# Kernel tuning notes

Measured on AMD Instinct MI355X. Metric: run time of the kernel, lower is better.

Reference implementation:

```python
import jax, jax.numpy as jnp
import numpy as np

N = 20000       # total atoms
E = 320000      # edges (avg degree 16)
F = 128         # num_features
R = 32          # num_radial
NB = 3          # num_blocks
CUTOFF = 5.0
MAX_Z = 37      # max_atomic_number + 1
MIN_DIST = 0.3
PI = 3.141592653589793


def swish(x):
    return x * jax.nn.sigmoid(x)


def sph_harm_l2(rhat):
    # Real spherical harmonics lmax=2, e3nn ordering, 'component' normalization.
    x, y, z = rhat[:, 0], rhat[:, 1], rhat[:, 2]
    s3, s5, s15 = 1.7320508075688772, 2.23606797749979, 3.872983346207417
    sh1 = jnp.stack([s3 * y, s3 * z, s3 * x], axis=-1)                    # l=1 (odd)
    sh2 = jnp.stack([s15 * x * y, s15 * y * z, 0.5 * s5 * (3.0 * z * z - 1.0),
                     s15 * z * x, 0.5 * s15 * (x * x - y * y)], axis=-1)  # l=2 (even)
    return sh1, sh2


def setup_inputs() -> dict:
    key = jax.random.key(0)
    ks = jax.random.split(key, 16)
    rn = lambda k, shape, scale: jax.random.normal(k, shape, dtype=jnp.float32) * scale
    inp = {}
    inp["z"] = jax.random.randint(ks[0], (N,), 0, MAX_Z)
    inp["pos"] = rn(ks[1], (N, 3), 3.0)
    inp["edge_index"] = jax.random.randint(ks[2], (2, E), 0, N)
    # embedding params
    inp["emb_table"] = rn(ks[3], (MAX_Z, F), 1.0)
    inp["emb_W"] = rn(ks[4], (F, F), F ** -0.5)
    inp["emb_b"] = jnp.zeros((F,), jnp.float32)
    # trainable Bessel frequencies (init n*pi, as in bessel RBF)
    inp["bessel_freq"] = jnp.arange(1, R + 1, dtype=jnp.float32) * PI
    # per-block params, stacked over NB blocks
    inp["Wf1"] = rn(ks[5], (NB, R, F), R ** -0.5)
    inp["bf1"] = jnp.zeros((NB, F), jnp.float32)
    inp["Wf2"] = rn(ks[6], (NB, F, 4 * F), F ** -0.5)
    inp["Wsrc"] = rn(ks[7], (NB, F, F), F ** -0.5)
    inp["Wu"] = rn(ks[8], (NB, F, 3 * F), F ** -0.5)
    inp["W1o"] = rn(ks[9], (NB, F, F), F ** -0.5)
    inp["W1e"] = rn(ks[10], (NB, F, F), F ** -0.5)
    inp["W2e"] = rn(ks[11], (NB, F, F), F ** -0.5)
    inp["Wup"] = rn(ks[12], (NB, 4 * F, F), (4 * F) ** -0.5)
    return inp


def forward(z, pos, edge_index, emb_table, emb_W, emb_b, bessel_freq,
            Wf1, bf1, Wf2, Wsrc, Wu, W1o, W1e, W2e, Wup):
    i, j = edge_index[0], edge_index[1]
    rij = pos[j] - pos[i]                                   # [E,3]
    r = jnp.sqrt(jnp.sum(rij * rij, axis=-1) + 1e-12)       # [E]
    rhat = rij / (r[:, None] + 1e-6)
    # mask replaces the edge filtering (min_distance and radius cutoff)
    edge_mask = ((r >= MIN_DIST) & (r < CUTOFF)).astype(pos.dtype)
    sh1, sh2 = sph_harm_l2(rhat)                            # [E,3], [E,5]
    # trainable Bessel RBF with cosine cutoff envelope
    fc = 0.5 * (jnp.cos(PI * r / CUTOFF) + 1.0) * edge_mask
    rbf = jnp.sqrt(2.0 / CUTOFF) * jnp.sin(bessel_freq[None, :] * r[:, None] / CUTOFF) / (r[:, None] + 1e-6)
    rbf = rbf * fc[:, None]                                 # [E,R]
    # atom embedding
    S = swish(emb_table[z] @ emb_W + emb_b)                 # [N,F]
    T = jnp.zeros((N, 11, F), S.dtype)                      # 1o(3)+1e(3)+2e(5) x F channels
    for b in range(NB):
        # radial filter network -> per-edge gates
        w = swish(rbf @ Wf1[b] + bf1[b]) @ Wf2[b]           # [E,4F]
        w = w * edge_mask[:, None]
        wS, w1, w2, w3 = jnp.split(w, 4, axis=-1)
        Sj = S[j]                                           # [E,F] gather
        # scalar messages
        mS = wS * swish(Sj @ Wsrc[b])                       # [E,F]
        aggS = jax.ops.segment_sum(mS, i, num_segments=N)   # [N,F]
        # equivariant messages: sh(l) outer-product edge features
        u1, u2, u3 = jnp.split(Sj @ Wu[b], 3, axis=-1)
        m1o = sh1[:, :, None] * (w1 * u1)[:, None, :]       # [E,3,F]
        m1e = sh1[:, :, None] * (w2 * u2)[:, None, :]       # [E,3,F]
        m2e = sh2[:, :, None] * (w3 * u3)[:, None, :]       # [E,5,F]
        mT = jnp.concatenate([m1o, m1e, m2e], axis=1)       # [E,11,F]
        aggT = jax.ops.segment_sum(mT, i, num_segments=N)   # [N,11,F] scatter-add
        Tin = T + aggT
        # per-irrep channel mixing (self-interaction)
        T1o = jnp.einsum('nmf,fg->nmg', Tin[:, 0:3], W1o[b])
        T1e = jnp.einsum('nmf,fg->nmg', Tin[:, 3:6], W1e[b])
        T2e = jnp.einsum('nmf,fg->nmg', Tin[:, 6:11], W2e[b])
        T = jnp.concatenate([T1o, T1e, T2e], axis=1)
        # invariant norms of each irrep feed back into scalar track
        inv = jnp.concatenate([jnp.sum(T1o * T1o, 1), jnp.sum(T1e * T1e, 1),
                               jnp.sum(T2e * T2e, 1)], axis=-1)   # [N,3F]
        S = S + swish(jnp.concatenate([aggS, inv], axis=-1) @ Wup[b])
    return S, T.reshape(N, 11 * F)


def reference(z, pos, edge_index, emb_table, emb_W, emb_b, bessel_freq,
              Wf1, bf1, Wf2, Wsrc, Wu, W1o, W1e, W2e, Wup):
    return forward(z, pos, edge_index, emb_table, emb_W, emb_b, bessel_freq,
                   Wf1, bf1, Wf2, Wsrc, Wu, W1o, W1e, W2e, Wup)
```

## Files before the change

### kernel.cpp

```cpp
#include <hip/hip_runtime.h>
#include <cstdint>
#include <cstddef>

#define NN 20000
#define EE 320000
#define FF 128
#define RR 32
#define MTE 16

typedef float  f32x4  __attribute__((ext_vector_type(4)));
typedef short  bf16x8 __attribute__((ext_vector_type(8)));

__device__ __forceinline__ float swishf(float x) {
    return x / (1.f + __expf(-x));
}
__device__ __forceinline__ unsigned short f2bf(float f) {
    unsigned int u = __builtin_bit_cast(unsigned int, f);
    u = (u + 0x7FFFu + ((u >> 16) & 1u)) >> 16;
    return (unsigned short)u;
}
__device__ __forceinline__ float bf2f(unsigned short h) {
    unsigned int u = ((unsigned int)h) << 16;
    return __builtin_bit_cast(float, u);
}

__global__ __launch_bounds__(256) void geom_deg_kernel(
    const float* __restrict__ pos, const int* __restrict__ eidx,
    int* __restrict__ deg)
{
    int e = blockIdx.x * 256 + threadIdx.x;
    if (e >= EE) return;
    int i = eidx[e], j = eidx[EE + e];
    float dx = pos[3*j+0] - pos[3*i+0];
    float dy = pos[3*j+1] - pos[3*i+1];
    float dz = pos[3*j+2] - pos[3*i+2];
    float r = sqrtf(dx*dx + dy*dy + dz*dz + 1e-12f);
    if (r >= 0.3f && r < 5.0f) atomicAdd(&deg[i], 1);
}

__global__ __launch_bounds__(256) void scan_kernel(
    const int* __restrict__ deg, int* __restrict__ cursor, int* __restrict__ cstart)
{
    __shared__ int part[256];
    const int t = threadIdx.x;
    const int lo = t * 79;
    const int hi = min(lo + 79, NN);
    int s = 0;
    for (int k = lo; k < hi; k++) s += deg[k];
    part[t] = s;
    __syncthreads();
    for (int off = 1; off < 256; off <<= 1) {
        int v = (t >= off) ? part[t - off] : 0;
        __syncthreads();
        part[t] += v;
        __syncthreads();
    }
    int run = (t == 0) ? 0 : part[t - 1];
    for (int k = lo; k < hi; k++) { cursor[k] = run; cstart[k] = run; run += deg[k]; }
    if (t == 255) cstart[NN] = part[255];
}

__global__ __launch_bounds__(256) void geom_scatter_kernel(
    const float* __restrict__ pos, const int* __restrict__ eidx,
    const float* __restrict__ freq, int* __restrict__ cursor,
    int* __restrict__ ei, int* __restrict__ ej,
    float* __restrict__ sh, unsigned short* __restrict__ rbfq)
{
    int e = blockIdx.x * 256 + threadIdx.x;
    if (e >= EE) return;
    int i = eidx[e], j = eidx[EE + e];
    float dx = pos[3*j+0] - pos[3*i+0];
    float dy = pos[3*j+1] - pos[3*i+1];
    float dz = pos[3*j+2] - pos[3*i+2];
    float r = sqrtf(dx*dx + dy*dy + dz*dz + 1e-12f);
    if (!(r >= 0.3f && r < 5.0f)) return;
    int slot = atomicAdd(&cursor[i], 1);
    ei[slot] = i; ej[slot] = j;
    float ir = 1.f / (r + 1e-6f);
    float x = dx*ir, y = dy*ir, z = dz*ir;
    const float s3 = 1.7320508075688772f, s5 = 2.23606797749979f, s15 = 3.872983346207417f;
    float* shp = sh + (size_t)slot * 8;
    shp[0] = s3*y; shp[1] = s3*z; shp[2] = s3*x;
    shp[3] = s15*x*y; shp[4] = s15*y*z; shp[5] = 0.5f*s5*(3.f*z*z - 1.f);
    shp[6] = s15*z*x; shp[7] = 0.5f*s15*(x*x - y*y);
    float fc = 0.5f * (cosf(3.14159265358979323846f * r * 0.2f) + 1.f);
    float pref = 0.6324555320336759f * fc * ir;
    unsigned short* rp = rbfq + (size_t)slot * RR;
    for (int k = 0; k < RR; k++) rp[k] = f2bf(pref * sinf(freq[k] * r * 0.2f));
}

__global__ __launch_bounds__(128) void embed_kernel(
    const int* __restrict__ z, const float* __restrict__ emb_table,
    const float* __restrict__ emb_W, const float* __restrict__ emb_b,
    float* __restrict__ S)
{
    int n = blockIdx.x;
    int f = threadIdx.x;
    __shared__ float row[FF];
    row[f] = emb_table[(size_t)z[n]*FF + f];
    __syncthreads();
    float acc = emb_b[f];
    for (int k = 0; k < FF; k++) acc += row[k] * emb_W[k*FF + f];
    S[(size_t)n*FF + f] = swishf(acc);
}

__global__ __launch_bounds__(256) void pack_kernel(
    const float* __restrict__ W1o, const float* __restrict__ W1e,
    const float* __restrict__ W2e, const float* __restrict__ Wup,
    unsigned short* __restrict__ ph, unsigned short* __restrict__ pl)
{
    int t = blockIdx.x * 256 + threadIdx.x;
    if (t >= 3 * 14336) return;
    int b = t / 14336, r = t % 14336;
    const float* src; int nks; size_t dstoff;
    if (r < 6144) {
        int mat = r / 2048, rr = r % 2048;
        src = (mat == 0 ? W1o : mat == 1 ? W1e : W2e) + (size_t)b * 16384;
        nks = 4;
        dstoff = (size_t)b * 114688 + (size_t)mat * 16384 + (size_t)rr * 8;
        r = rr;
    } else {
        int rr = r - 6144;
        src = Wup + (size_t)b * 65536;
        nks = 16;
        dstoff = (size_t)b * 114688 + 49152 + (size_t)rr * 8;
        r = rr;
    }
    int lane = r & 63;
    int fi = r >> 6;
    int ks = fi % nks, ct = fi / nks;
    int col = ct * 16 + (lane & 15);
    int kb = ks * 32 + (lane >> 4) * 8;
    #pragma unroll
    for (int e = 0; e < 8; e++) {
        float v = src[(size_t)(kb + e) * 128 + col];
        unsigned short h = f2bf(v);
        ph[dstoff + e] = h;
        pl[dstoff + e] = f2bf(v - bf2f(h));
    }
}

__global__ __launch_bounds__(256) void pack_pu_kernel(
    const float* __restrict__ Wsrc, const float* __restrict__ Wu,
    unsigned short* __restrict__ packPU)
{
    int t = blockIdx.x * 256 + threadIdx.x;
    if (t >= 3 * 8192) return;
    int b = t / 8192, r = t % 8192;
    int lane = r & 63, fi = r >> 6;
    int ks = fi & 3, ct = fi >> 2;
    int kb = ks * 32 + (lane >> 4) * 8;
    int colq = lane & 15;
    const float* src; int col, stride;
    if (ct < 8) { src = Wsrc + (size_t)b * 16384; col = ct*16 + colq; stride = 128; }
    else        { src = Wu   + (size_t)b * 49152; col = (ct-8)*16 + colq; stride = 384; }
    size_t dst = (size_t)b * 65536 + (size_t)fi * 512 + (size_t)lane * 8;
    #pragma unroll
    for (int e = 0; e < 8; e++)
        packPU[dst + e] = f2bf(src[(size_t)(kb + e) * stride + col]);
}

__global__ __launch_bounds__(256) void pack_f2_kernel(
    const float* __restrict__ Wf2, unsigned short* __restrict__ packF2)
{
    int t = blockIdx.x * 256 + threadIdx.x;
    if (t >= 3 * 8192) return;
    int b = t / 8192, r = t % 8192;
    int lane = r & 63, fi = r >> 6;
    int ks = fi & 3, ct = fi >> 2;
    int kb = ks * 32 + (lane >> 4) * 8;
    int col = ct * 16 + (lane & 15);
    const float* src = Wf2 + (size_t)b * 65536;
    size_t dst = (size_t)b * 65536 + (size_t)fi * 512 + (size_t)lane * 8;
    #pragma unroll
    for (int e = 0; e < 8; e++)
        packF2[dst + e] = f2bf(src[(size_t)(kb + e) * 512 + col]);
}

__global__ __launch_bounds__(256) void proj_kernel(
    const float* __restrict__ S, const unsigned short* __restrict__ packPU,
    unsigned short* __restrict__ PU)
{
    __shared__ float stage[16][132];
    const int tid = threadIdx.x;
    const int n0 = blockIdx.x * 16;

    for (int idx = tid; idx < 512; idx += 256) {
        int row = idx >> 5, k4 = (idx & 31) << 2;
        *(float4*)&stage[row][k4] = *(const float4*)&S[((size_t)(n0 + row) << 7) + k4];
    }
    __syncthreads();

    const int lane = tid & 63;
    const int wid  = tid >> 6;
    const int row  = lane & 15;
    const int k0   = (lane >> 4) * 8;

    f32x4 acc[8];
    #pragma unroll
    for (int c = 0; c < 8; c++) acc[c] = (f32x4){0.f, 0.f, 0.f, 0.f};

    #pragma unroll
    for (int ks = 0; ks < 4; ks++) {
        const float* sp = &stage[row][ks*32 + k0];
        bf16x8 a;
        #pragma unroll
        for (int e = 0; e < 8; e++) a[e] = (short)f2bf(sp[e]);
        #pragma unroll
        for (int cti = 0; cti < 8; cti++) {
            int ct = wid * 8 + cti;
            bf16x8 b = *(const bf16x8*)(packPU + (((size_t)ct * 4 + ks) * 64 + lane) * 8);
            acc[cti] = __builtin_amdgcn_mfma_f32_16x16x32_bf16(a, b, acc[cti], 0, 0, 0);
        }
    }

    #pragma unroll
    for (int cti = 0; cti < 8; cti++) {
        int ct = wid * 8 + cti;
        int cblk = ct >> 3;
        int fcol = (ct & 7) * 16 + (lane & 15);
        #pragma unroll
        for (int q = 0; q < 4; q++) {
            int n = n0 + (lane >> 4) * 4 + q;
            float v = acc[cti][q];
            if (cblk == 0) v = swishf(v);
            PU[(size_t)n * 512 + fcol * 4 + cblk] = f2bf(v);
        }
    }
}

__global__ __launch_bounds__(256) void msg_kernel(
    const int* __restrict__ cstart,
    const int* __restrict__ ei, const int* __restrict__ ej,
    const float* __restrict__ sh, const unsigned short* __restrict__ rbfq,
    const float* __restrict__ Wf1, const float* __restrict__ bf1,
    const unsigned short* __restrict__ packF2, const unsigned short* __restrict__ PU,
    float* __restrict__ aggS, float* __restrict__ aggT)
{
    const int Ea = cstart[NN];
    const int base = blockIdx.x * MTE;
    if (base >= Ea) return;
    const int nval = min(MTE, Ea - base);
    const int tid = threadIdx.x;
    const int f = tid & 127;
    const int half = tid >> 7;
    const int lane = tid & 63;
    const int wid  = tid >> 6;

    __shared__ float          rbf_s[MTE][RR];
    __shared__ unsigned short h_s[MTE][FF];
    __shared__ unsigned short w_s[MTE][520];
    __shared__ float          sh_s[MTE][8];
    __shared__ int            i_s[MTE], j_s[MTE];

    if (tid < MTE) {
        i_s[tid] = (tid < nval) ? ei[base + tid] : -1;
        j_s[tid] = (tid < nval) ? ej[base + tid] : 0;
    }
    if (tid >= 64 && tid < 64 + MTE*8) {
        int t = tid - 64, e = t >> 3;
        sh_s[e][t & 7] = (e < nval) ? sh[(size_t)(base + e)*8 + (t & 7)] : 0.f;
    }
    for (int t = tid; t < MTE*RR; t += 256) {
        int e = t >> 5, k = t & 31;
        rbf_s[e][k] = (e < nval) ? bf2f(rbfq[(size_t)(base + e)*RR + k]) : 0.f;
    }
    __syncthreads();

    {
        float hacc[8];
        float bb = bf1[f];
        #pragma unroll
        for (int k = 0; k < 8; k++) hacc[k] = bb;
        for (int r = 0; r < RR; r++) {
            float wv = Wf1[r*FF + f];
            #pragma unroll
            for (int k = 0; k < 8; k++) hacc[k] += rbf_s[half*8 + k][r] * wv;
        }
        #pragma unroll
        for (int k = 0; k < 8; k++)
            h_s[half*8 + k][f] = f2bf(swishf(hacc[k]));
    }
    __syncthreads();

    {
        const int ra = lane & 15, k0 = (lane >> 4) * 8;
        f32x4 wacc[8];
        #pragma unroll
        for (int c = 0; c < 8; c++) wacc[c] = (f32x4){0.f, 0.f, 0.f, 0.f};
        #pragma unroll
        for (int ks = 0; ks < 4; ks++) {
            bf16x8 a = *(const bf16x8*)&h_s[ra][ks*32 + k0];
            #pragma unroll
            for (int cti = 0; cti < 8; cti++) {
                int ct = wid * 8 + cti;
                bf16x8 b = *(const bf16x8*)(packF2 + (((size_t)ct * 4 + ks) * 64 + lane) * 8);
                wacc[cti] = __builtin_amdgcn_mfma_f32_16x16x32_bf16(a, b, wacc[cti], 0, 0, 0);
            }
        }
        #pragma unroll
        for (int cti = 0; cti < 8; cti++) {
            int ct = wid * 8 + cti;
            int cblk = ct >> 3;
            int fcol = (ct & 7) * 16 + (lane & 15);
            #pragma unroll
            for (int q = 0; q < 4; q++)
                w_s[(lane >> 4)*4 + q][fcol*4 + cblk] = f2bf(wacc[cti][q]);
        }
    }
    __syncthreads();

    float aS=0.f, a3=0.f, a4=0.f, a5=0.f;
    float a0=0.f,a1=0.f,a2=0.f,a6=0.f,a7=0.f,a8=0.f,a9=0.f,a10=0.f;
    int cur = i_s[0];

    auto flush = [&](int node) {
        bool interior = (cstart[node] >= base) && (cstart[node + 1] <= base + nval);
        if (half == 0) {
            size_t sA = ((size_t)node << 7) + f;
            size_t bT = (((size_t)node*11 + 3) << 7) + f;
            if (interior) {
                aggS[sA] = aS;
                aggT[bT] = a3; aggT[bT + 128] = a4; aggT[bT + 256] = a5;
            } else {
                atomicAdd(&aggS[sA], aS);
                atomicAdd(&aggT[bT], a3); atomicAdd(&aggT[bT + 128], a4); atomicAdd(&aggT[bT + 256], a5);
            }
            aS = a3 = a4 = a5 = 0.f;
        } else {
            size_t bT  = (((size_t)node*11) << 7) + f;
            size_t bT2 = (((size_t)node*11 + 6) << 7) + f;
            if (interior) {
                aggT[bT] = a0; aggT[bT + 128] = a1; aggT[bT + 256] = a2;
                aggT[bT2] = a6; aggT[bT2 + 128] = a7; aggT[bT2 + 256] = a8;
                aggT[bT2 + 384] = a9; aggT[bT2 + 512] = a10;
            } else {
                atomicAdd(&aggT[bT], a0); atomicAdd(&aggT[bT + 128], a1); atomicAdd(&aggT[bT + 256], a2);
                atomicAdd(&aggT[bT2], a6); atomicAdd(&aggT[bT2 + 128], a7); atomicAdd(&aggT[bT2 + 256], a8);
                atomicAdd(&aggT[bT2 + 384], a9); atomicAdd(&aggT[bT2 + 512], a10);
            }
            a0=a1=a2=a6=a7=a8=a9=a10=0.f;
        }
    };

    #pragma unroll
    for (int e = 0; e < MTE; e++) {
        if (e >= nval) break;
        int ie = i_s[e];
        if (ie != cur) { flush(cur); cur = ie; }
        uint2 wv2 = *(const uint2*)&w_s[e][f*4];
        uint2 pv  = *(const uint2*)(PU + ((size_t)j_s[e] << 9) + (f << 2));
        if (half == 0) {
            float wS = bf2f((unsigned short)(wv2.x & 0xffff));
            float w2 = bf2f((unsigned short)(wv2.y & 0xffff));
            float P  = bf2f((unsigned short)(pv.x  & 0xffff));
            float U2 = bf2f((unsigned short)(pv.y  & 0xffff));
            aS += wS * P;
            float v = w2 * U2;
            a3 += sh_s[e][0]*v; a4 += sh_s[e][1]*v; a5 += sh_s[e][2]*v;
        } else {
            float w1 = bf2f((unsigned short)(wv2.x >> 16));
            float w3 = bf2f((unsigned short)(wv2.y >> 16));
            float U1 = bf2f((unsigned short)(pv.x  >> 16));
            float U3 = bf2f((unsigned short)(pv.y  >> 16));
            float v1 = w1 * U1;
            a0 += sh_s[e][0]*v1; a1 += sh_s[e][1]*v1; a2 += sh_s[e][2]*v1;
            float v3 = w3 * U3;
            a6 += sh_s[e][3]*v3; a7 += sh_s[e][4]*v3; a8 += sh_s[e][5]*v3;
            a9 += sh_s[e][6]*v3; a10 += sh_s[e][7]*v3;
        }
    }
    flush(cur);
}

template<int GSIZE>
__global__ __launch_bounds__(256) void tgemm_kernel(
    const float* __restrict__ aggT,
    const unsigned short* __restrict__ Wh, const unsigned short* __restrict__ Wl,
    float* __restrict__ T, float* __restrict__ inv,
    int goff, int invoff, int addT)
{
    __shared__ float stage[GSIZE][16][132];
    const int tid = threadIdx.x;
    const int n0 = blockIdx.x * 16;

    const int total = GSIZE * 16 * 32;
    for (int idx = tid; idx < total; idx += 256) {
        int mg  = idx >> 9;
        int rem = idx & 511;
        int row = rem >> 5;
        int k4  = (rem & 31) << 2;
        size_t g = (((size_t)(n0 + row) * 11 + goff + mg) << 7) + k4;
        float4 v = *(const float4*)&aggT[g];
        if (addT) {
            float4 tv = *(const float4*)&T[g];
            v.x += tv.x; v.y += tv.y; v.z += tv.z; v.w += tv.w;
        }
        *(float4*)&stage[mg][row][k4] = v;
    }
    __syncthreads();

    const int lane = tid & 63;
    const int wid  = tid >> 6;
    const int row  = lane & 15;
    const int k0   = (lane >> 4) * 8;

    f32x4 acc[GSIZE][2];
    #pragma unroll
    for (int mg = 0; mg < GSIZE; mg++) {
        acc[mg][0] = (f32x4){0.f, 0.f, 0.f, 0.f};
        acc[mg][1] = (f32x4){0.f, 0.f, 0.f, 0.f};
    }

    #pragma unroll
    for (int ks = 0; ks < 4; ks++) {
        bf16x8 ah[GSIZE], al[GSIZE];
        #pragma unroll
        for (int mg = 0; mg < GSIZE; mg++) {
            const float* sp = &stage[mg][row][ks*32 + k0];
            float v0[4], v1[4];
            *(float4*)v0 = *(const float4*)sp;
            *(float4*)v1 = *(const float4*)(sp + 4);
            #pragma unroll
            for (int e = 0; e < 4; e++) {
                unsigned short h0 = f2bf(v0[e]);
                ah[mg][e]   = (short)h0;
                al[mg][e]   = (short)f2bf(v0[e] - bf2f(h0));
                unsigned short h1 = f2bf(v1[e]);
                ah[mg][4+e] = (short)h1;
                al[mg][4+e] = (short)f2bf(v1[e] - bf2f(h1));
            }
        }
        #pragma unroll
        for (int cti = 0; cti < 2; cti++) {
            const int ct = wid * 2 + cti;
            size_t boff = (((size_t)ct * 4 + ks) * 64 + lane) * 8;
            bf16x8 bh = *(const bf16x8*)(Wh + boff);
            bf16x8 bl = *(const bf16x8*)(Wl + boff);
            #pragma unroll
            for (int mg = 0; mg < GSIZE; mg++) {
                acc[mg][cti] = __builtin_amdgcn_mfma_f32_16x16x32_bf16(ah[mg], bh, acc[mg][cti], 0, 0, 0);
                acc[mg][cti] = __builtin_amdgcn_mfma_f32_16x16x32_bf16(al[mg], bh, acc[mg][cti], 0, 0, 0);
                acc[mg][cti] = __builtin_amdgcn_mfma_f32_16x16x32_bf16(ah[mg], bl, acc[mg][cti], 0, 0, 0);
            }
        }
    }

    #pragma unroll
    for (int cti = 0; cti < 2; cti++) {
        const int ct = wid * 2 + cti;
        const int fc = ct * 16 + (lane & 15);
        #pragma unroll
        for (int q = 0; q < 4; q++) {
            const int n = n0 + (lane >> 4) * 4 + q;
            float iv = 0.f;
            #pragma unroll
            for (int mg = 0; mg < GSIZE; mg++) {
                float o = acc[mg][cti][q];
                T[(((size_t)n * 11 + goff + mg) << 7) + fc] = o;
                iv += o * o;
            }
            inv[(size_t)n * 384 + invoff + fc] = iv;
        }
    }
}

__global__ __launch_bounds__(256) void sgemm2_kernel(
    const float* __restrict__ aggS, const float* __restrict__ inv,
    const unsigned short* __restrict__ Wh, const unsigned short* __restrict__ Wl,
    float* __restrict__ S)
{
    __shared__ float stage[16][516];
    const int tid = threadIdx.x;
    const int n0 = blockIdx.x * 16;

    for (int idx = tid; idx < 16 * 128; idx += 256) {
        int row = idx >> 7;
        int k4  = (idx & 127) << 2;
        float4 v;
        if (k4 < 128) v = *(const float4*)&aggS[((size_t)(n0 + row) << 7) + k4];
        else          v = *(const float4*)&inv[(size_t)(n0 + row) * 384 + (k4 - 128)];
        *(float4*)&stage[row][k4] = v;
    }
    __syncthreads();

    const int lane = tid & 63;
    const int wid  = tid >> 6;
    const int row  = lane & 15;
    const int k0   = (lane >> 4) * 8;

    f32x4 acc[2];
    acc[0] = (f32x4){0.f, 0.f, 0.f, 0.f};
    acc[1] = (f32x4){0.f, 0.f, 0.f, 0.f};

    for (int ks = 0; ks < 16; ks++) {
        const float* sp = &stage[row][ks*32 + k0];
        float v0[4], v1[4];
        *(float4*)v0 = *(const float4*)sp;
        *(float4*)v1 = *(const float4*)(sp + 4);
        bf16x8 ah, al;
        #pragma unroll
        for (int e = 0; e < 4; e++) {
            unsigned short h0 = f2bf(v0[e]);
            ah[e]   = (short)h0;
            al[e]   = (short)f2bf(v0[e] - bf2f(h0));
            unsigned short h1 = f2bf(v1[e]);
            ah[4+e] = (short)h1;
            al[4+e] = (short)f2bf(v1[e] - bf2f(h1));
        }
        #pragma unroll
        for (int cti = 0; cti < 2; cti++) {
            const int ct = wid * 2 + cti;
            size_t boff = (((size_t)ct * 16 + ks) * 64 + lane) * 8;
            bf16x8 bh = *(const bf16x8*)(Wh + boff);
            bf16x8 bl = *(const bf16x8*)(Wl + boff);
            acc[cti] = __builtin_amdgcn_mfma_f32_16x16x32_bf16(ah, bh, acc[cti], 0, 0, 0);
            acc[cti] = __builtin_amdgcn_mfma_f32_16x16x32_bf16(al, bh, acc[cti], 0, 0, 0);
            acc[cti] = __builtin_amdgcn_mfma_f32_16x16x32_bf16(ah, bl, acc[cti], 0, 0, 0);
        }
    }

    #pragma unroll
    for (int cti = 0; cti < 2; cti++) {
        const int ct = wid * 2 + cti;
        const int fc = ct * 16 + (lane & 15);
        #pragma unroll
        for (int q = 0; q < 4; q++) {
            const int n = n0 + (lane >> 4) * 4 + q;
            size_t o = ((size_t)n << 7) + fc;
            S[o] += swishf(acc[cti][q]);
        }
    }
}

extern "C" void kernel_launch(void* const* d_in, const int* in_sizes, int n_in,
                              void* d_out, int out_size, void* d_ws, size_t ws_size,
                              hipStream_t stream)
{
    const int*   z         = (const int*)  d_in[0];
    const float* pos       = (const float*)d_in[1];
    const int*   eidx      = (const int*)  d_in[2];
    const float* emb_table = (const float*)d_in[3];
    const float* emb_W     = (const float*)d_in[4];
    const float* emb_b     = (const float*)d_in[5];
    const float* freq      = (const float*)d_in[6];
    const float* Wf1       = (const float*)d_in[7];
    const float* bf1       = (const float*)d_in[8];
    const float* Wf2       = (const float*)d_in[9];
    const float* Wsrc      = (const float*)d_in[10];
    const float* Wu        = (const float*)d_in[11];
    const float* W1o       = (const float*)d_in[12];
    const float* W1e       = (const float*)d_in[13];
    const float* W2e       = (const float*)d_in[14];
    const float* Wup       = (const float*)d_in[15];

    float* S = (float*)d_out;
    float* T = S + (size_t)NN*FF;

    char* w = (char*)d_ws;
    int*   deg    = (int*)w;                      w += (size_t)NN*4 + 128;
    int*   cursor = (int*)w;                      w += (size_t)NN*4 + 128;
    int*   cstart = (int*)w;                      w += (size_t)(NN+1)*4 + 124;
    int*   ei     = (int*)w;                      w += (size_t)EE*4;
    int*   ej     = (int*)w;                      w += (size_t)EE*4;
    float* sh     = (float*)w;                    w += (size_t)EE*8*4;
    unsigned short* rbfq = (unsigned short*)w;    w += (size_t)EE*RR*2;
    unsigned short* PU   = (unsigned short*)w;    w += (size_t)NN*512*2;
    float* aggS   = (float*)w;                    w += (size_t)NN*FF*4;
    float* aggT   = (float*)w;                    w += (size_t)NN*11*FF*4;
    float* inv    = (float*)w;                    w += (size_t)NN*384*4;
    unsigned short* packH  = (unsigned short*)w;  w += (size_t)344064*2;
    unsigned short* packL  = (unsigned short*)w;  w += (size_t)344064*2;
    unsigned short* packPU = (unsigned short*)w;  w += (size_t)3*65536*2;
    unsigned short* packF2 = (unsigned short*)w;  w += (size_t)3*65536*2;

    hipMemsetAsync(deg, 0, (size_t)NN*4, stream);

    geom_deg_kernel<<<(EE + 255)/256, 256, 0, stream>>>(pos, eidx, deg);
    scan_kernel<<<1, 256, 0, stream>>>(deg, cursor, cstart);
    geom_scatter_kernel<<<(EE + 255)/256, 256, 0, stream>>>(pos, eidx, freq, cursor, ei, ej, sh, rbfq);
    embed_kernel<<<NN, 128, 0, stream>>>(z, emb_table, emb_W, emb_b, S);
    pack_kernel<<<(3*14336 + 255)/256, 256, 0, stream>>>(W1o, W1e, W2e, Wup, packH, packL);
    pack_pu_kernel<<<(3*8192 + 255)/256, 256, 0, stream>>>(Wsrc, Wu, packPU);
    pack_f2_kernel<<<(3*8192 + 255)/256, 256, 0, stream>>>(Wf2, packF2);

    for (int b = 0; b < 3; b++) {
        hipMemsetAsync(aggS, 0, (size_t)NN*FF*4 + (size_t)NN*11*FF*4, stream);
        proj_kernel<<<NN/16, 256, 0, stream>>>(S, packPU + (size_t)b*65536, PU);
        msg_kernel<<<(EE + MTE - 1)/MTE, 256, 0, stream>>>(
            cstart, ei, ej, sh, rbfq,
            Wf1 + (size_t)b*RR*FF, bf1 + (size_t)b*FF,
            packF2 + (size_t)b*65536, PU, aggS, aggT);

        const unsigned short* H = packH + (size_t)b*114688;
        const unsigned short* L = packL + (size_t)b*114688;
        tgemm_kernel<3><<<NN/16, 256, 0, stream>>>(aggT, H +     0, L +     0, T, inv, 0,   0, b > 0);
        tgemm_kernel<3><<<NN/16, 256, 0, stream>>>(aggT, H + 16384, L + 16384, T, inv, 3, 128, b > 0);
        tgemm_kernel<5><<<NN/16, 256, 0, stream>>>(aggT, H + 32768, L + 32768, T, inv, 6, 256, b > 0);
        sgemm2_kernel<<<NN/16, 256, 0, stream>>>(aggS, inv, H + 49152, L + 49152, S);
    }
}
```

Measured before the change: 998.2 us.

## Fuse next-block projection into sgemm2, clear only boundary aggregates, prefetch PU rows

New measurement: 1.268 ms. +27.1%, slower.

```diff
diff --git a/kernel.cpp b/kernel.cpp
--- a/kernel.cpp
+++ b/kernel.cpp
@@ -58,6 +58,33 @@
     int run = (t == 0) ? 0 : part[t - 1];
     for (int k = lo; k < hi; k++) { cursor[k] = run; cstart[k] = run; run += deg[k]; }
     if (t == 255) cstart[NN] = part[255];
+}
+
+__global__ __launch_bounds__(256) void clearlist_kernel(
+    const int* __restrict__ cstart, int* __restrict__ list, int* __restrict__ cnt)
+{
+    int n = blockIdx.x * 256 + threadIdx.x;
+    if (n >= NN) return;
+    int s = cstart[n], t = cstart[n + 1];
+    bool need = (s == t) || ((s >> 4) != ((t - 1) >> 4));
+    if (need) list[atomicAdd(cnt, 1)] = n;
+}
+
+__global__ __launch_bounds__(256) void clear_kernel(
+    const int* __restrict__ list, const int* __restrict__ cnt,
+    float* __restrict__ aggS, float* __restrict__ aggT)
+{
+    const int total = (*cnt) * 384;
+    const f32x4 z = (f32x4){0.f, 0.f, 0.f, 0.f};
+    for (int idx = blockIdx.x * 256 + threadIdx.x; idx < total; idx += gridDim.x * 256) {
+        int ni = idx / 384, rem = idx - ni * 384;
+        int n = list[ni];
+        if (rem < 32) *(f32x4*)&aggS[((size_t)n << 7) + rem * 4] = z;
+        else {
+            int r = rem - 32;
+            *(f32x4*)&aggT[(((size_t)n * 11 + (r >> 5)) << 7) + (r & 31) * 4] = z;
+        }
+    }
 }
 
 __global__ __launch_bounds__(256) void geom_scatter_kernel(
@@ -310,6 +337,12 @@
     }
     __syncthreads();
 
+    uint2 puv[MTE];
+    #pragma unroll
+    for (int e = 0; e < MTE; e++)
+        puv[e] = *(const uint2*)(PU + ((size_t)j_s[e] << 9) + (f << 2));
+    __builtin_amdgcn_sched_barrier(0);
+
     float aS=0.f, a3=0.f, a4=0.f, a5=0.f;
     float a0=0.f,a1=0.f,a2=0.f,a6=0.f,a7=0.f,a8=0.f,a9=0.f,a10=0.f;
     int cur = i_s[0];
@@ -349,7 +382,7 @@
         int ie = i_s[e];
         if (ie != cur) { flush(cur); cur = ie; }
         uint2 wv2 = *(const uint2*)&w_s[e][f*4];
-        uint2 pv  = *(const uint2*)(PU + ((size_t)j_s[e] << 9) + (f << 2));
+        uint2 pv  = puv[e];
         if (half == 0) {
             float wS = bf2f((unsigned short)(wv2.x & 0xffff));
             float w2 = bf2f((unsigned short)(wv2.y & 0xffff));
@@ -468,9 +501,11 @@
 __global__ __launch_bounds__(256) void sgemm2_kernel(
     const float* __restrict__ aggS, const float* __restrict__ inv,
     const unsigned short* __restrict__ Wh, const unsigned short* __restrict__ Wl,
-    float* __restrict__ S)
+    const unsigned short* __restrict__ packPUn,
+    float* __restrict__ S, unsigned short* __restrict__ PU, int doPU)
 {
     __shared__ float stage[16][516];
+    __shared__ float snew[16][132];
     const int tid = threadIdx.x;
     const int n0 = blockIdx.x * 16;
 
@@ -528,7 +563,44 @@
         for (int q = 0; q < 4; q++) {
             const int n = n0 + (lane >> 4) * 4 + q;
             size_t o = ((size_t)n << 7) + fc;
-            S[o] += swishf(acc[cti][q]);
+            float sv = S[o] + swishf(acc[cti][q]);
+            S[o] = sv;
+            snew[(lane >> 4)*4 + q][fc] = sv;
+        }
+    }
+
+    if (!doPU) return;
+    __syncthreads();
+
+    {
+        f32x4 pacc[8];
+        #pragma unroll
+        for (int c = 0; c < 8; c++) pacc[c] = (f32x4){0.f, 0.f, 0.f, 0.f};
+        #pragma unroll
+        for (int ks = 0; ks < 4; ks++) {
+            bf16x8 a;
+            #pragma unroll
+            for (int e = 0; e < 8; e++)
+                a[e] = (short)f2bf(snew[row][ks*32 + k0 + e]);
+            #pragma unroll
+            for (int cti = 0; cti < 8; cti++) {
+                int ct = wid * 8 + cti;
+                bf16x8 b = *(const bf16x8*)(packPUn + (((size_t)ct * 4 + ks) * 64 + lane) * 8);
+                pacc[cti] = __builtin_amdgcn_mfma_f32_16x16x32_bf16(a, b, pacc[cti], 0, 0, 0);
+            }
+        }
+        #pragma unroll
+        for (int cti = 0; cti < 8; cti++) {
+            int ct = wid * 8 + cti;
+            int cblk = ct >> 3;
+            int fcol = (ct & 7) * 16 + (lane & 15);
+            #pragma unroll
+            for (int q = 0; q < 4; q++) {
+                int n = n0 + (lane >> 4) * 4 + q;
+                float v = pacc[cti][q];
+                if (cblk == 0) v = swishf(v);
+                PU[((size_t)n << 9) + fcol*4 + cblk] = f2bf(v);
+            }
         }
     }
 }
@@ -558,35 +630,40 @@
     float* T = S + (size_t)NN*FF;
 
     char* w = (char*)d_ws;
-    int*   deg    = (int*)w;                      w += (size_t)NN*4 + 128;
-    int*   cursor = (int*)w;                      w += (size_t)NN*4 + 128;
-    int*   cstart = (int*)w;                      w += (size_t)(NN+1)*4 + 124;
-    int*   ei     = (int*)w;                      w += (size_t)EE*4;
-    int*   ej     = (int*)w;                      w += (size_t)EE*4;
-    float* sh     = (float*)w;                    w += (size_t)EE*8*4;
+    int*   deg     = (int*)w;                     w += (size_t)NN*4 + 128;
+    int*   cursor  = (int*)w;                     w += (size_t)NN*4 + 128;
+    int*   cstart  = (int*)w;                     w += (size_t)(NN+1)*4 + 124;
+    int*   clearcnt= (int*)w;                     w += 128;
+    int*   clearlist=(int*)w;                     w += (size_t)NN*4 + 128;
+    int*   ei      = (int*)w;                     w += (size_t)EE*4;
+    int*   ej      = (int*)w;                     w += (size_t)EE*4;
+    float* sh      = (float*)w;                   w += (size_t)EE*8*4;
     unsigned short* rbfq = (unsigned short*)w;    w += (size_t)EE*RR*2;
     unsigned short* PU   = (unsigned short*)w;    w += (size_t)NN*512*2;
-    float* aggS   = (float*)w;                    w += (size_t)NN*FF*4;
-    float* aggT   = (float*)w;                    w += (size_t)NN*11*FF*4;
-    float* inv    = (float*)w;                    w += (size_t)NN*384*4;
+    float* aggS    = (float*)w;                   w += (size_t)NN*FF*4;
+    float* aggT    = (float*)w;                   w += (size_t)NN*11*FF*4;
+    float* inv     = (float*)w;                   w += (size_t)NN*384*4;
     unsigned short* packH  = (unsigned short*)w;  w += (size_t)344064*2;
     unsigned short* packL  = (unsigned short*)w;  w += (size_t)344064*2;
     unsigned short* packPU = (unsigned short*)w;  w += (size_t)3*65536*2;
     unsigned short* packF2 = (unsigned short*)w;  w += (size_t)3*65536*2;
 
     hipMemsetAsync(deg, 0, (size_t)NN*4, stream);
+    hipMemsetAsync(clearcnt, 0, 4, stream);
 
     geom_deg_kernel<<<(EE + 255)/256, 256, 0, stream>>>(pos, eidx, deg);
     scan_kernel<<<1, 256, 0, stream>>>(deg, cursor, cstart);
+    clearlist_kernel<<<(NN + 255)/256, 256, 0, stream>>>(cstart, clearlist, clearcnt);
     geom_scatter_kernel<<<(EE + 255)/256, 256, 0, stream>>>(pos, eidx, freq, cursor, ei, ej, sh, rbfq);
     embed_kernel<<<NN, 128, 0, stream>>>(z, emb_table, emb_W, emb_b, S);
     pack_kernel<<<(3*14336 + 255)/256, 256, 0, stream>>>(W1o, W1e, W2e, Wup, packH, packL);
     pack_pu_kernel<<<(3*8192 + 255)/256, 256, 0, stream>>>(Wsrc, Wu, packPU);
     pack_f2_kernel<<<(3*8192 + 255)/256, 256, 0, stream>>>(Wf2, packF2);
 
+    proj_kernel<<<NN/16, 256, 0, stream>>>(S, packPU, PU);
+
     for (int b = 0; b < 3; b++) {
-        hipMemsetAsync(aggS, 0, (size_t)NN*FF*4 + (size_t)NN*11*FF*4, stream);
-        proj_kernel<<<NN/16, 256, 0, stream>>>(S, packPU + (size_t)b*65536, PU);
+        clear_kernel<<<2048, 256, 0, stream>>>(clearlist, clearcnt, aggS, aggT);
         msg_kernel<<<(EE + MTE - 1)/MTE, 256, 0, stream>>>(
             cstart, ei, ej, sh, rbfq,
             Wf1 + (size_t)b*RR*FF, bf1 + (size_t)b*FF,
@@ -597,6 +674,9 @@
         tgemm_kernel<3><<<NN/16, 256, 0, stream>>>(aggT, H +     0, L +     0, T, inv, 0,   0, b > 0);
         tgemm_kernel<3><<<NN/16, 256, 0, stream>>>(aggT, H + 16384, L + 16384, T, inv, 3, 128, b > 0);
         tgemm_kernel<5><<<NN/16, 256, 0, stream>>>(aggT, H + 32768, L + 32768, T, inv, 6, 256, b > 0);
-        sgemm2_kernel<<<NN/16, 256, 0, stream>>>(aggS, inv, H + 49152, L + 49152, S);
-    }
-}
+        sgemm2_kernel<<<NN/16, 256, 0, stream>>>(
+            aggS, inv, H + 49152, L + 49152,
+            packPU + (size_t)(b < 2 ? (b+1)*65536 : 0),
+            S, PU, b < 2);
+    }
+}
```
